# Optimization experiments

Hardware: AMD Instinct MI355X
Metric: run time of the kernel (lower is better)

Reference implementation:

```python
import jax, jax.numpy as jnp
import numpy as np

B, T, I, H = 256, 1024, 128, 256


def setup_inputs() -> dict:
    key = jax.random.key(0)
    ks = jax.random.split(key, 10)
    p = lambda k, shape: jax.random.normal(k, shape, dtype=jnp.float32) * 0.1
    return {
        "x": jax.random.normal(ks[0], (B, T, I), dtype=jnp.float32),
        # forget gate
        "f_wh": p(ks[1], (H, H)), "f_wx": p(ks[2], (I, H)), "f_b": p(ks[3], (H,)),
        # input (create) gate: potential (tanh) and percent (sigmoid) branches
        "i_wh_pot": p(ks[4], (H, H)), "i_wx_pot": p(ks[5], (I, H)), "i_b_pot": p(ks[6], (H,)),
        "i_wh_perc": p(ks[7], (H, H)), "i_wx_perc": p(ks[8], (I, H)), "i_b_perc": p(ks[9], (H,)),
        # output gate
        "o_wh": p(jax.random.fold_in(key, 10), (H, H)),
        "o_wx": p(jax.random.fold_in(key, 11), (I, H)),
        "o_b": p(jax.random.fold_in(key, 12), (H,)),
    }


def reference(x, f_wh, f_wx, f_b, i_wh_pot, i_wx_pot, i_b_pot,
              i_wh_perc, i_wx_perc, i_b_perc, o_wh, o_wx, o_b):
    # x: [B, T, I]
    sigmoid, tanh = jax.nn.sigmoid, jnp.tanh

    def step(carry, xt):  # xt: [B, I]
        s, l = carry  # short_term [B,H], long_term [B,H]
        forget = sigmoid(s @ f_wh + xt @ f_wx + f_b)
        create = sigmoid(s @ i_wh_perc + xt @ i_wx_perc + i_b_perc) * \
                 tanh(s @ i_wh_pot + xt @ i_wx_pot + i_b_pot)
        l_new = forget * l + create
        s_new = tanh(l_new) * sigmoid(s @ o_wh + xt @ o_wx + o_b)
        return (s_new, l_new), None

    init = (jnp.zeros((x.shape[0], f_b.shape[0]), x.dtype),
            jnp.zeros((x.shape[0], f_b.shape[0]), x.dtype))
    (short_term, long_term), _ = jax.lax.scan(step, init, jnp.swapaxes(x, 0, 1))
    return short_term, long_term
```

## Files before the change

### kernel.cpp

```cpp
#include <hip/hip_runtime.h>
#include <cstdint>

#define T_STEPS 1024
#define I_DIM 128
#define H_DIM 256

typedef __attribute__((ext_vector_type(8))) short bf16x8;
typedef __attribute__((ext_vector_type(4))) float f32x4;

__device__ __forceinline__ uint32_t f2bf(float f) {
    uint32_t u = __builtin_bit_cast(uint32_t, f);
    return (u + 0x7FFFu + ((u >> 16) & 1u)) >> 16;
}
__device__ __forceinline__ uint32_t pk2bf(float lo, float hi) {
    return (f2bf(lo) & 0xFFFFu) | (f2bf(hi) << 16);
}
__device__ __forceinline__ float sigmoid_(float v) { return 1.f / (1.f + __expf(-v)); }
__device__ __forceinline__ float tanh_(float v) { float e = __expf(2.f * v); return 1.f - 2.f / (e + 1.f); }

__global__ void __launch_bounds__(256, 1)
lstm_kernel(const float* __restrict__ x,
            const float* __restrict__ f_wh, const float* __restrict__ f_wx, const float* __restrict__ f_b,
            const float* __restrict__ p_wh, const float* __restrict__ p_wx, const float* __restrict__ p_b,
            const float* __restrict__ c_wh, const float* __restrict__ c_wx, const float* __restrict__ c_b,
            const float* __restrict__ o_wh, const float* __restrict__ o_wx, const float* __restrict__ o_b,
            float* __restrict__ out, uint32_t* __restrict__ flags, uint32_t* __restrict__ sbuf)
{
    __shared__ __align__(16) uint8_t lds[65536];
    uint8_t* WH = lds;
    uint8_t* WX = lds + 32768;
    uint8_t* SL = lds + 49152;
    uint8_t* XT = lds + 57344;
    float*   GB = (float*)(lds + 61440);

    const int tid  = (int)threadIdx.x;
    const int lane = tid & 63;
    const int wv   = tid >> 6;
    const int blk  = (int)blockIdx.x;
    const int grp  = blk & 15;
    const int cwg  = blk >> 4;
    const int grow0 = grp << 4;
    const int hc0   = cwg << 4;

    uint32_t* gflags = flags + grp * 32;

    const float* wh = (wv == 0) ? f_wh : (wv == 1) ? p_wh : (wv == 2) ? c_wh : o_wh;
    const float* wx = (wv == 0) ? f_wx : (wv == 1) ? p_wx : (wv == 2) ? c_wx : o_wx;
    const float* bp = (wv == 0) ? f_b  : (wv == 1) ? p_b  : (wv == 2) ? c_b  : o_b;

    {
        const int col = lane & 15, kc = lane >> 4;
        const uint32_t csw = (uint32_t)((col & 7) << 4);
        uint8_t* whb = WH + (size_t)(wv * 16 + col) * 512;
        #pragma unroll
        for (int it = 0; it < 8; ++it) {
            const int k0 = it * 32 + kc * 8;
            float v0 = wh[(size_t)(k0 + 0) * H_DIM + hc0 + col];
            float v1 = wh[(size_t)(k0 + 1) * H_DIM + hc0 + col];
            float v2 = wh[(size_t)(k0 + 2) * H_DIM + hc0 + col];
            float v3 = wh[(size_t)(k0 + 3) * H_DIM + hc0 + col];
            float v4 = wh[(size_t)(k0 + 4) * H_DIM + hc0 + col];
            float v5 = wh[(size_t)(k0 + 5) * H_DIM + hc0 + col];
            float v6 = wh[(size_t)(k0 + 6) * H_DIM + hc0 + col];
            float v7 = wh[(size_t)(k0 + 7) * H_DIM + hc0 + col];
            uint4 pk;
            pk.x = pk2bf(v0, v1); pk.y = pk2bf(v2, v3);
            pk.z = pk2bf(v4, v5); pk.w = pk2bf(v6, v7);
            *(uint4*)(whb + (((uint32_t)(it * 64 + kc * 16)) ^ csw)) = pk;
        }
        uint8_t* wxb = WX + (size_t)(wv * 16 + col) * 256;
        #pragma unroll
        for (int it = 0; it < 4; ++it) {
            const int k0 = it * 32 + kc * 8;
            float v0 = wx[(size_t)(k0 + 0) * H_DIM + hc0 + col];
            float v1 = wx[(size_t)(k0 + 1) * H_DIM + hc0 + col];
            float v2 = wx[(size_t)(k0 + 2) * H_DIM + hc0 + col];
            float v3 = wx[(size_t)(k0 + 3) * H_DIM + hc0 + col];
            float v4 = wx[(size_t)(k0 + 4) * H_DIM + hc0 + col];
            float v5 = wx[(size_t)(k0 + 5) * H_DIM + hc0 + col];
            float v6 = wx[(size_t)(k0 + 6) * H_DIM + hc0 + col];
            float v7 = wx[(size_t)(k0 + 7) * H_DIM + hc0 + col];
            uint4 pk;
            pk.x = pk2bf(v0, v1); pk.y = pk2bf(v2, v3);
            pk.z = pk2bf(v4, v5); pk.w = pk2bf(v6, v7);
            *(uint4*)(wxb + (((uint32_t)(it * 64 + kc * 16)) ^ csw)) = pk;
        }
    }
    const float bias = bp[hc0 + (lane & 15)];

    const int crow = tid >> 4, ccol = tid & 15;
    const uint32_t pub_idx = (uint32_t)(grow0 + crow) * 128u + (uint32_t)cwg * 8u + (uint32_t)(ccol >> 1);

    if ((tid & 1) == 0)
        __hip_atomic_store(sbuf + pub_idx, 0u, __ATOMIC_RELAXED, __HIP_MEMORY_SCOPE_SYSTEM);
    asm volatile("s_waitcnt vmcnt(0)" ::: "memory");
    __syncthreads();
    if (tid == 0)
        __hip_atomic_store(gflags + cwg, 1u, __ATOMIC_RELAXED, __HIP_MEMORY_SCOPE_SYSTEM);

    const int xrow = tid >> 4, xseg = tid & 15;
    const uint32_t xsw = (uint32_t)((xrow & 7) << 4);
    const float* xptr = x + (size_t)(grow0 + xrow) * (T_STEPS * I_DIM) + xseg * 8;
    float4 xr0 = *(const float4*)(xptr);
    float4 xr1 = *(const float4*)(xptr + 4);

    const int fr = lane & 15, fkc = lane >> 4;
    const uint32_t fsw = (uint32_t)((fr & 7) << 4);
    uint8_t* slA = SL + (size_t)fr * 512;
    uint8_t* xtA = XT + (size_t)fr * 256;
    uint8_t* whB = WH + (size_t)(wv * 16 + fr) * 512;
    uint8_t* wxB = WX + (size_t)(wv * 16 + fr) * 256;

    uint32_t* myflag = gflags + xseg;

    float l_reg = 0.f, s_fin = 0.f, l_fin = 0.f;

    for (int t = 0; t < T_STEPS; ++t) {
        {
            uint4 pk;
            pk.x = pk2bf(xr0.x, xr0.y); pk.y = pk2bf(xr0.z, xr0.w);
            pk.z = pk2bf(xr1.x, xr1.y); pk.w = pk2bf(xr1.z, xr1.w);
            *(uint4*)(XT + (size_t)xrow * 256 + (((uint32_t)(xseg * 16)) ^ xsw)) = pk;
        }
        {
            const int tn = (t + 1 < T_STEPS) ? (t + 1) : (T_STEPS - 1);
            const float* p = xptr + (size_t)tn * I_DIM;
            xr0 = *(const float4*)(p);
            xr1 = *(const float4*)(p + 4);
        }
        __syncthreads();

        {
            const uint32_t target = (uint32_t)t + 1u;
            while (__hip_atomic_load(myflag, __ATOMIC_RELAXED, __HIP_MEMORY_SCOPE_SYSTEM) < target) {}
        }
        asm volatile("" ::: "memory");
        uint4 g0, g1;
        {
            const uint32_t* src = sbuf + (size_t)(t & 1) * 32768 + (size_t)(grow0 + xrow) * 128 + xseg * 8;
            asm volatile("global_load_dwordx4 %0, %1, off sc0 sc1" : "=v"(g0) : "v"(src) : "memory");
            asm volatile("global_load_dwordx4 %0, %1, off offset:16 sc0 sc1" : "=v"(g1) : "v"(src) : "memory");
        }
        f32x4 acc = {0.f, 0.f, 0.f, 0.f};
        #pragma unroll
        for (int q = 0; q < 4; ++q) {
            const uint32_t o = (uint32_t)(q * 64 + fkc * 16);
            uint4 av = *(const uint4*)(xtA + (o ^ fsw));
            uint4 bv = *(const uint4*)(wxB + (o ^ fsw));
            acc = __builtin_amdgcn_mfma_f32_16x16x32_bf16(
                __builtin_bit_cast(bf16x8, av), __builtin_bit_cast(bf16x8, bv), acc, 0, 0, 0);
        }
        asm volatile("s_waitcnt vmcnt(0)" ::: "memory");
        __builtin_amdgcn_sched_barrier(0);
        {
            uint8_t* dst = SL + (size_t)xrow * 512;
            const uint32_t o = (uint32_t)(xseg * 32);
            *(uint4*)(dst + (o ^ xsw)) = g0;
            *(uint4*)(dst + ((o + 16) ^ xsw)) = g1;
        }
        __syncthreads();
        #pragma unroll
        for (int q = 0; q < 8; ++q) {
            const uint32_t o = (uint32_t)(q * 64 + fkc * 16);
            uint4 av = *(const uint4*)(slA + (o ^ fsw));
            uint4 bv = *(const uint4*)(whB + (o ^ fsw));
            acc = __builtin_amdgcn_mfma_f32_16x16x32_bf16(
                __builtin_bit_cast(bf16x8, av), __builtin_bit_cast(bf16x8, bv), acc, 0, 0, 0);
        }
        #pragma unroll
        for (int j = 0; j < 4; ++j) {
            const float pre = acc[j] + bias;
            const float a = (wv == 1) ? tanh_(pre) : sigmoid_(pre);
            GB[wv * 256 + (fkc * 4 + j) * 16 + fr] = a;
        }
        __syncthreads();
        {
            const float fg  = GB[0 * 256 + crow * 16 + ccol];
            const float pot = GB[1 * 256 + crow * 16 + ccol];
            const float prc = GB[2 * 256 + crow * 16 + ccol];
            const float og  = GB[3 * 256 + crow * 16 + ccol];
            const float lnew = fg * l_reg + prc * pot;
            const float snew = tanh_(lnew) * og;
            l_reg = lnew;
            if (t == T_STEPS - 1) { s_fin = snew; l_fin = lnew; }
            const uint32_t sb = f2bf(snew);
            const uint32_t ob = (uint32_t)__shfl_xor((int)sb, 1, 64);
            if (((tid & 1) == 0) && (t != T_STEPS - 1)) {
                const uint32_t pkd = (sb & 0xFFFFu) | (ob << 16);
                __hip_atomic_store(sbuf + (size_t)((t + 1) & 1) * 32768 + pub_idx, pkd,
                                   __ATOMIC_RELAXED, __HIP_MEMORY_SCOPE_SYSTEM);
            }
        }
        if (t != T_STEPS - 1) {
            asm volatile("s_waitcnt vmcnt(0)" ::: "memory");
            __syncthreads();
            if (tid == 0)
                __hip_atomic_store(gflags + cwg, (uint32_t)t + 2u,
                                   __ATOMIC_RELAXED, __HIP_MEMORY_SCOPE_SYSTEM);
        }
    }

    out[(size_t)(grow0 + crow) * H_DIM + hc0 + ccol] = s_fin;
    out[(size_t)H_DIM * H_DIM + (size_t)(grow0 + crow) * H_DIM + hc0 + ccol] = l_fin;
}

extern "C" void kernel_launch(void* const* d_in, const int* in_sizes, int n_in,
                              void* d_out, int out_size, void* d_ws, size_t ws_size,
                              hipStream_t stream) {
    const float* x    = (const float*)d_in[0];
    const float* f_wh = (const float*)d_in[1];
    const float* f_wx = (const float*)d_in[2];
    const float* f_b  = (const float*)d_in[3];
    const float* p_wh = (const float*)d_in[4];
    const float* p_wx = (const float*)d_in[5];
    const float* p_b  = (const float*)d_in[6];
    const float* c_wh = (const float*)d_in[7];
    const float* c_wx = (const float*)d_in[8];
    const float* c_b  = (const float*)d_in[9];
    const float* o_wh = (const float*)d_in[10];
    const float* o_wx = (const float*)d_in[11];
    const float* o_b  = (const float*)d_in[12];
    float* outp = (float*)d_out;
    uint32_t* flags = (uint32_t*)d_ws;
    uint32_t* sbuf  = (uint32_t*)((char*)d_ws + 4096);

    hipMemsetAsync(d_ws, 0, 4096, stream);

    void* args[] = { (void*)&x,
                     (void*)&f_wh, (void*)&f_wx, (void*)&f_b,
                     (void*)&p_wh, (void*)&p_wx, (void*)&p_b,
                     (void*)&c_wh, (void*)&c_wx, (void*)&c_b,
                     (void*)&o_wh, (void*)&o_wx, (void*)&o_b,
                     (void*)&outp, (void*)&flags, (void*)&sbuf };
    hipLaunchCooperativeKernel((const void*)lstm_kernel, dim3(256), dim3(256), args, 0, stream);
}
```

Baseline: 2.301 ms.

## Replace per-block flag barrier with step-tagged state words and register-resident weights

Each published bf16 pair of the hidden state is now stored together with its timestep tag in one 8-byte write. Consumers poll the data itself until every tag matches, which removes the separate flag store, the vmcnt wait, the extra __syncthreads, and the flag spin per step. Weight B-fragments are hoisted from LDS into registers once before the loop, and the recurrent MFMA chain is split into two accumulators to shorten the dependency chain. The gate buffer gets padded strides to avoid LDS bank conflicts. The cost is doubled exchange traffic, more polling loads hitting the shared buffer, higher register pressure, and a larger workspace memset.

Result: faster. 1.947 ms (-15.4%).

```diff
diff --git a/kernel.cpp b/kernel.cpp
--- a/kernel.cpp
+++ b/kernel.cpp
@@ -7,6 +7,7 @@
 
 typedef __attribute__((ext_vector_type(8))) short bf16x8;
 typedef __attribute__((ext_vector_type(4))) float f32x4;
+typedef __attribute__((ext_vector_type(2))) unsigned int u32x2;
 
 __device__ __forceinline__ uint32_t f2bf(float f) {
     uint32_t u = __builtin_bit_cast(uint32_t, f);
@@ -24,9 +25,9 @@
             const float* __restrict__ p_wh, const float* __restrict__ p_wx, const float* __restrict__ p_b,
             const float* __restrict__ c_wh, const float* __restrict__ c_wx, const float* __restrict__ c_b,
             const float* __restrict__ o_wh, const float* __restrict__ o_wx, const float* __restrict__ o_b,
-            float* __restrict__ out, uint32_t* __restrict__ flags, uint32_t* __restrict__ sbuf)
+            float* __restrict__ out, uint8_t* __restrict__ ws)
 {
-    __shared__ __align__(16) uint8_t lds[65536];
+    __shared__ __align__(16) uint8_t lds[65792];
     uint8_t* WH = lds;
     uint8_t* WX = lds + 32768;
     uint8_t* SL = lds + 49152;
@@ -42,7 +43,7 @@
     const int grow0 = grp << 4;
     const int hc0   = cwg << 4;
 
-    uint32_t* gflags = flags + grp * 32;
+    uint8_t* sbase = ws + 4096;
 
     const float* wh = (wv == 0) ? f_wh : (wv == 1) ? p_wh : (wv == 2) ? c_wh : o_wh;
     const float* wx = (wv == 0) ? f_wx : (wv == 1) ? p_wx : (wv == 2) ? c_wx : o_wx;
@@ -87,16 +88,30 @@
         }
     }
     const float bias = bp[hc0 + (lane & 15)];
+    __syncthreads();
+
+    const int fr = lane & 15, fkc = lane >> 4;
+    const uint32_t fsw = (uint32_t)((fr & 7) << 4);
+    uint8_t* slA = SL + (size_t)fr * 512;
+    uint8_t* xtA = XT + (size_t)fr * 256;
+    const uint8_t* whB = WH + (size_t)(wv * 16 + fr) * 512;
+    const uint8_t* wxB = WX + (size_t)(wv * 16 + fr) * 256;
+
+    uint4 bwh[8], bwx[4];
+    #pragma unroll
+    for (int q = 0; q < 8; ++q)
+        bwh[q] = *(const uint4*)(whB + (((uint32_t)(q * 64 + fkc * 16)) ^ fsw));
+    #pragma unroll
+    for (int q = 0; q < 4; ++q)
+        bwx[q] = *(const uint4*)(wxB + (((uint32_t)(q * 64 + fkc * 16)) ^ fsw));
 
     const int crow = tid >> 4, ccol = tid & 15;
-    const uint32_t pub_idx = (uint32_t)(grow0 + crow) * 128u + (uint32_t)cwg * 8u + (uint32_t)(ccol >> 1);
-
-    if ((tid & 1) == 0)
-        __hip_atomic_store(sbuf + pub_idx, 0u, __ATOMIC_RELAXED, __HIP_MEMORY_SCOPE_SYSTEM);
-    asm volatile("s_waitcnt vmcnt(0)" ::: "memory");
-    __syncthreads();
-    if (tid == 0)
-        __hip_atomic_store(gflags + cwg, 1u, __ATOMIC_RELAXED, __HIP_MEMORY_SCOPE_SYSTEM);
+
+    if ((tid & 1) == 0) {
+        uint8_t* pdst = sbase + (size_t)(grow0 + crow) * 1024 + (size_t)(cwg * 8 + (ccol >> 1)) * 8;
+        u32x2 pd; pd.x = 0u; pd.y = 1u;
+        asm volatile("global_store_dwordx2 %0, %1, off sc0 sc1" :: "v"(pdst), "v"(pd) : "memory");
+    }
 
     const int xrow = tid >> 4, xseg = tid & 15;
     const uint32_t xsw = (uint32_t)((xrow & 7) << 4);
@@ -104,15 +119,6 @@
     float4 xr0 = *(const float4*)(xptr);
     float4 xr1 = *(const float4*)(xptr + 4);
 
-    const int fr = lane & 15, fkc = lane >> 4;
-    const uint32_t fsw = (uint32_t)((fr & 7) << 4);
-    uint8_t* slA = SL + (size_t)fr * 512;
-    uint8_t* xtA = XT + (size_t)fr * 256;
-    uint8_t* whB = WH + (size_t)(wv * 16 + fr) * 512;
-    uint8_t* wxB = WX + (size_t)(wv * 16 + fr) * 256;
-
-    uint32_t* myflag = gflags + xseg;
-
     float l_reg = 0.f, s_fin = 0.f, l_fin = 0.f;
 
     for (int t = 0; t < T_STEPS; ++t) {
@@ -130,55 +136,68 @@
         }
         __syncthreads();
 
-        {
-            const uint32_t target = (uint32_t)t + 1u;
-            while (__hip_atomic_load(myflag, __ATOMIC_RELAXED, __HIP_MEMORY_SCOPE_SYSTEM) < target) {}
-        }
-        asm volatile("" ::: "memory");
-        uint4 g0, g1;
-        {
-            const uint32_t* src = sbuf + (size_t)(t & 1) * 32768 + (size_t)(grow0 + xrow) * 128 + xseg * 8;
-            asm volatile("global_load_dwordx4 %0, %1, off sc0 sc1" : "=v"(g0) : "v"(src) : "memory");
-            asm volatile("global_load_dwordx4 %0, %1, off offset:16 sc0 sc1" : "=v"(g1) : "v"(src) : "memory");
-        }
-        f32x4 acc = {0.f, 0.f, 0.f, 0.f};
+        f32x4 accA = {0.f, 0.f, 0.f, 0.f};
         #pragma unroll
         for (int q = 0; q < 4; ++q) {
-            const uint32_t o = (uint32_t)(q * 64 + fkc * 16);
-            uint4 av = *(const uint4*)(xtA + (o ^ fsw));
-            uint4 bv = *(const uint4*)(wxB + (o ^ fsw));
-            acc = __builtin_amdgcn_mfma_f32_16x16x32_bf16(
-                __builtin_bit_cast(bf16x8, av), __builtin_bit_cast(bf16x8, bv), acc, 0, 0, 0);
-        }
-        asm volatile("s_waitcnt vmcnt(0)" ::: "memory");
-        __builtin_amdgcn_sched_barrier(0);
-        {
+            uint4 av = *(const uint4*)(xtA + (((uint32_t)(q * 64 + fkc * 16)) ^ fsw));
+            accA = __builtin_amdgcn_mfma_f32_16x16x32_bf16(
+                __builtin_bit_cast(bf16x8, av), __builtin_bit_cast(bf16x8, bwx[q]), accA, 0, 0, 0);
+        }
+
+        uint4 g0, g1, g2, g3;
+        uint32_t m;
+        const uint32_t e = (uint32_t)t + 1u;
+        const uint8_t* src = sbase + (size_t)((t & 1) ? 262144 : 0)
+                           + (size_t)(grow0 + xrow) * 1024 + (size_t)xseg * 64;
+        do {
+            asm volatile("global_load_dwordx4 %0, %1, off sc0 sc1"
+                         : "=v"(g0) : "v"(src) : "memory");
+            asm volatile("global_load_dwordx4 %0, %1, off offset:16 sc0 sc1"
+                         : "=v"(g1) : "v"(src) : "memory");
+            asm volatile("global_load_dwordx4 %0, %1, off offset:32 sc0 sc1"
+                         : "=v"(g2) : "v"(src) : "memory");
+            asm volatile("global_load_dwordx4 %0, %1, off offset:48 sc0 sc1"
+                         : "=v"(g3) : "v"(src) : "memory");
+            asm volatile("s_waitcnt vmcnt(0)" ::: "memory");
+            __builtin_amdgcn_sched_barrier(0);
+            m = (g0.y ^ e) | (g0.w ^ e) | (g1.y ^ e) | (g1.w ^ e)
+              | (g2.y ^ e) | (g2.w ^ e) | (g3.y ^ e) | (g3.w ^ e);
+        } while (m != 0);
+
+        {
+            uint4 d0; d0.x = g0.x; d0.y = g0.z; d0.z = g1.x; d0.w = g1.z;
+            uint4 d1; d1.x = g2.x; d1.y = g2.z; d1.z = g3.x; d1.w = g3.z;
             uint8_t* dst = SL + (size_t)xrow * 512;
             const uint32_t o = (uint32_t)(xseg * 32);
-            *(uint4*)(dst + (o ^ xsw)) = g0;
-            *(uint4*)(dst + ((o + 16) ^ xsw)) = g1;
+            *(uint4*)(dst + (o ^ xsw)) = d0;
+            *(uint4*)(dst + ((o + 16) ^ xsw)) = d1;
         }
         __syncthreads();
-        #pragma unroll
-        for (int q = 0; q < 8; ++q) {
-            const uint32_t o = (uint32_t)(q * 64 + fkc * 16);
-            uint4 av = *(const uint4*)(slA + (o ^ fsw));
-            uint4 bv = *(const uint4*)(whB + (o ^ fsw));
-            acc = __builtin_amdgcn_mfma_f32_16x16x32_bf16(
-                __builtin_bit_cast(bf16x8, av), __builtin_bit_cast(bf16x8, bv), acc, 0, 0, 0);
-        }
+
+        f32x4 accB = {0.f, 0.f, 0.f, 0.f};
+        #pragma unroll
+        for (int q = 0; q < 4; ++q) {
+            uint4 a0 = *(const uint4*)(slA + (((uint32_t)(q * 64 + fkc * 16)) ^ fsw));
+            uint4 a1 = *(const uint4*)(slA + (((uint32_t)((q + 4) * 64 + fkc * 16)) ^ fsw));
+            accA = __builtin_amdgcn_mfma_f32_16x16x32_bf16(
+                __builtin_bit_cast(bf16x8, a0), __builtin_bit_cast(bf16x8, bwh[q]), accA, 0, 0, 0);
+            accB = __builtin_amdgcn_mfma_f32_16x16x32_bf16(
+                __builtin_bit_cast(bf16x8, a1), __builtin_bit_cast(bf16x8, bwh[q + 4]), accB, 0, 0, 0);
+        }
+
         #pragma unroll
         for (int j = 0; j < 4; ++j) {
-            const float pre = acc[j] + bias;
+            const float pre = accA[j] + accB[j] + bias;
             const float a = (wv == 1) ? tanh_(pre) : sigmoid_(pre);
-            GB[wv * 256 + (fkc * 4 + j) * 16 + fr] = a;
+            GB[wv * 272 + (fkc * 4 + j) * 17 + fr] = a;
         }
         __syncthreads();
-        {
-            const float fg  = GB[0 * 256 + crow * 16 + ccol];
-            const float pot = GB[1 * 256 + crow * 16 + ccol];
-            const float prc = GB[2 * 256 + crow * 16 + ccol];
-            const float og  = GB[3 * 256 + crow * 16 + ccol];
+
+        {
+            const float fg  = GB[0 * 272 + crow * 17 + ccol];
+            const float pot = GB[1 * 272 + crow * 17 + ccol];
+            const float prc = GB[2 * 272 + crow * 17 + ccol];
+            const float og  = GB[3 * 272 + crow * 17 + ccol];
             const float lnew = fg * l_reg + prc * pot;
             const float snew = tanh_(lnew) * og;
             l_reg = lnew;
@@ -186,17 +205,11 @@
             const uint32_t sb = f2bf(snew);
             const uint32_t ob = (uint32_t)__shfl_xor((int)sb, 1, 64);
             if (((tid & 1) == 0) && (t != T_STEPS - 1)) {
-                const uint32_t pkd = (sb & 0xFFFFu) | (ob << 16);
-                __hip_atomic_store(sbuf + (size_t)((t + 1) & 1) * 32768 + pub_idx, pkd,
-                                   __ATOMIC_RELAXED, __HIP_MEMORY_SCOPE_SYSTEM);
+                uint8_t* pdst = sbase + (size_t)(((t + 1) & 1) ? 262144 : 0)
+                              + (size_t)(grow0 + crow) * 1024 + (size_t)(cwg * 8 + (ccol >> 1)) * 8;
+                u32x2 pd; pd.x = (sb & 0xFFFFu) | (ob << 16); pd.y = (uint32_t)t + 2u;
+                asm volatile("global_store_dwordx2 %0, %1, off sc0 sc1" :: "v"(pdst), "v"(pd) : "memory");
             }
-        }
-        if (t != T_STEPS - 1) {
-            asm volatile("s_waitcnt vmcnt(0)" ::: "memory");
-            __syncthreads();
-            if (tid == 0)
-                __hip_atomic_store(gflags + cwg, (uint32_t)t + 2u,
-                                   __ATOMIC_RELAXED, __HIP_MEMORY_SCOPE_SYSTEM);
         }
     }
 
@@ -221,16 +234,15 @@
     const float* o_wx = (const float*)d_in[11];
     const float* o_b  = (const float*)d_in[12];
     float* outp = (float*)d_out;
-    uint32_t* flags = (uint32_t*)d_ws;
-    uint32_t* sbuf  = (uint32_t*)((char*)d_ws + 4096);
-
-    hipMemsetAsync(d_ws, 0, 4096, stream);
+    uint8_t* wsp = (uint8_t*)d_ws;
+
+    hipMemsetAsync(d_ws, 0, 4096 + 2 * 262144, stream);
 
     void* args[] = { (void*)&x,
                      (void*)&f_wh, (void*)&f_wx, (void*)&f_b,
                      (void*)&p_wh, (void*)&p_wx, (void*)&p_b,
                      (void*)&c_wh, (void*)&c_wx, (void*)&c_b,
                      (void*)&o_wh, (void*)&o_wx, (void*)&o_b,
-                     (void*)&outp, (void*)&flags, (void*)&sbuf };
+                     (void*)&outp, (void*)&wsp };
     hipLaunchCooperativeKernel((const void*)lstm_kernel, dim3(256), dim3(256), args, 0, stream);
 }
```
